# Kernel optimization log

Hardware: AMD Instinct MI355X
Metric: run time of the kernel (lower is better)

The kernel has to match this reference:

```python
import jax, jax.numpy as jnp
import numpy as np

N_NODES = 100000
N_EDGES = 3200000
D_FEAT = 512
D_HID = 64
D_LAT = 16
N_CLASS = 10
N_FLOW = 10
K_PROP = 10
ALPHA_TELEPORT = 0.1


def setup_inputs() -> dict:
    key = jax.random.key(0)
    ks = jax.random.split(key, 8)
    x = jax.random.normal(ks[0], (N_NODES, D_FEAT), jnp.float32)
    edge_index = jax.random.randint(ks[1], (2, N_EDGES), 0, N_NODES)
    p_c = jax.random.uniform(ks[2], (N_CLASS,), jnp.float32) + 0.1
    p_c = p_c / p_c.sum()
    W1 = jax.random.normal(ks[3], (D_FEAT, D_HID), jnp.float32) / np.sqrt(D_FEAT).astype(np.float32)
    b1 = jnp.zeros((D_HID,), jnp.float32)
    W2 = jax.random.normal(ks[4], (D_HID, D_LAT), jnp.float32) / np.sqrt(D_HID).astype(np.float32)
    b2 = jnp.zeros((D_LAT,), jnp.float32)
    flow_z0 = jax.random.normal(ks[5], (N_FLOW, N_CLASS, D_LAT), jnp.float32) * 0.1
    flow_alpha_prime = jax.random.normal(ks[6], (N_FLOW, N_CLASS, 1), jnp.float32) * 0.1
    flow_beta = jax.random.normal(ks[7], (N_FLOW, N_CLASS, 1), jnp.float32) * 0.1
    return dict(x=x, edge_index=edge_index, p_c=p_c, W1=W1, b1=b1, W2=W2, b2=b2,
                flow_z0=flow_z0, flow_alpha_prime=flow_alpha_prime, flow_beta=flow_beta)


def _batched_radial_log_prob(z, flow_z0, flow_alpha_prime, flow_beta):
    # Per-class batched radial flow (invertible pyro-style parameterization).
    # z: [N, D] -> log_q: [N, C]
    C, D = flow_z0.shape[1], flow_z0.shape[2]
    zz = jnp.broadcast_to(z[None], (C, z.shape[0], D))  # [C, N, D]
    sum_logdet = jnp.zeros((C, z.shape[0]), z.dtype)
    for l in range(flow_z0.shape[0]):  # small fixed number of flow layers
        z0 = flow_z0[l][:, None, :]                               # [C,1,D]
        alpha = jax.nn.softplus(flow_alpha_prime[l])[:, None, :]  # [C,1,1]
        beta_hat = -alpha + jax.nn.softplus(flow_beta[l])[:, None, :]
        dz = zz - z0
        r = jnp.sqrt(jnp.sum(dz * dz, axis=-1, keepdims=True))    # [C,N,1]
        h = 1.0 / (alpha + r)
        bh = beta_hat * h
        zz = zz + bh * dz
        logdet = (D - 1) * jnp.log1p(bh) + jnp.log1p(bh - beta_hat * r * h * h)
        sum_logdet = sum_logdet + logdet[..., 0]
    log_base = -0.5 * jnp.sum(zz * zz, axis=-1) - 0.5 * D * jnp.log(2.0 * jnp.pi)
    return (log_base + sum_logdet).T  # [N, C]


def _appnp(beta_ft, edge_index, n_nodes):
    # APPNP with self loops and symmetric gcn normalization over edge list.
    src = jnp.concatenate([edge_index[0], jnp.arange(n_nodes)])
    dst = jnp.concatenate([edge_index[1], jnp.arange(n_nodes)])
    deg = jax.ops.segment_sum(jnp.ones_like(src, dtype=beta_ft.dtype), dst, num_segments=n_nodes)
    dinv = jnp.where(deg > 0, jax.lax.rsqrt(jnp.maximum(deg, 1.0)), 0.0)
    norm = (dinv[src] * dinv[dst])[:, None]  # [E+N, 1]
    x0 = beta_ft
    b = beta_ft
    for _ in range(K_PROP):
        agg = jax.ops.segment_sum(norm * b[src], dst, num_segments=n_nodes)
        b = (1.0 - ALPHA_TELEPORT) * agg + ALPHA_TELEPORT * x0
    return b


def reference(x, edge_index, p_c, W1, b1, W2, b2, flow_z0, flow_alpha_prime, flow_beta):
    h = jax.nn.relu(x @ W1 + b1)           # input_encoder (dropout inactive at eval)
    z = h @ W2 + b2                        # latent_encoder, [N, D_LAT]
    log_q = _batched_radial_log_prob(z, flow_z0, flow_alpha_prime, flow_beta)
    log_q_per_class = log_q + jnp.log(p_c)[None, :]
    log_scale = 0.5 * D_LAT * jnp.log(4.0 * jnp.pi)  # 'latent-new' evidence scale
    beta_ft = jnp.exp(jnp.clip(log_q_per_class + log_scale, -30.0, 30.0))
    beta = _appnp(beta_ft, edge_index, x.shape[0])
    alpha = 1.0 + beta
    soft = alpha / jnp.sum(alpha, axis=-1, keepdims=True)
    hard = jnp.argmax(soft, axis=-1)
    return hard[:, None], soft
```

## Files before the change

kernel.cpp:

```cpp
#include <hip/hip_runtime.h>
#include <math.h>
#include <limits.h>

#define DF 512
#define DH 64
#define DL 16
#define NC 10
#define NF 10
#define KPROP 10

#define BSH 7
#define BW  (1 << BSH)
#define MAXB 1024
#define TILE 16384

__device__ __forceinline__ float softplus_(float x){
  return fmaxf(x, 0.0f) + log1pf(expf(-fabsf(x)));
}

__device__ __forceinline__ unsigned int f2bf_(float f){
  unsigned int u = __float_as_uint(f);
  return (u + 0x7FFFu + ((u >> 16) & 1u)) >> 16;
}
__device__ __forceinline__ unsigned int pack2bf_(float lo, float hi){
  return f2bf_(lo) | (f2bf_(hi) << 16);
}

#define BM 64
#define BN 64
#define BK 32
__global__ __launch_bounds__(256) void k_gemm1z(const float* __restrict__ x,
    const float* __restrict__ W1, const float* __restrict__ b1,
    const float* __restrict__ W2, const float* __restrict__ b2,
    float* __restrict__ z, int N)
{
  __shared__ float smem[2*BK*(BM+4)];
  float (*At)[BM+4] = (float(*)[BM+4])smem;
  float (*Bs)[BN+4] = (float(*)[BN+4])(smem + BK*(BM+4));
  __shared__ float W2s[DH][DL];
  __shared__ float b2s[DL];
  const int tid = threadIdx.x;
  for (int i = tid; i < DH*DL; i += 256) W2s[i>>4][i&15] = W2[i];
  if (tid < DL) b2s[tid] = b2[tid];
  const int tx = tid & 15, ty = tid >> 4;
  const int row0 = blockIdx.x * BM;
  float acc[4][4] = {};
  for (int k0 = 0; k0 < DF; k0 += BK) {
    #pragma unroll
    for (int i = 0; i < 2; ++i) {
      int idx = tid + i*256;
      int r  = idx >> 3;
      int kk = (idx & 7) << 2;
      int row = row0 + r;
      float4 va = make_float4(0.f,0.f,0.f,0.f);
      if (row < N) va = *(const float4*)&x[(size_t)row*DF + k0 + kk];
      At[kk+0][r]=va.x; At[kk+1][r]=va.y; At[kk+2][r]=va.z; At[kk+3][r]=va.w;
      int r2 = idx >> 4;
      int c4 = (idx & 15) << 2;
      float4 vb = *(const float4*)&W1[(size_t)(k0+r2)*DH + c4];
      Bs[r2][c4+0]=vb.x; Bs[r2][c4+1]=vb.y; Bs[r2][c4+2]=vb.z; Bs[r2][c4+3]=vb.w;
    }
    __syncthreads();
    #pragma unroll
    for (int kk = 0; kk < BK; ++kk) {
      float4 av = *(const float4*)&At[kk][ty<<2];
      float4 bv = *(const float4*)&Bs[kk][tx<<2];
      float a4[4]={av.x,av.y,av.z,av.w};
      float b4[4]={bv.x,bv.y,bv.z,bv.w};
      #pragma unroll
      for (int i=0;i<4;++i)
        #pragma unroll
        for (int j=0;j<4;++j) acc[i][j] = fmaf(a4[i], b4[j], acc[i][j]);
    }
    __syncthreads();
  }
  float4 bias = ((const float4*)b1)[tx];
  float bias4[4] = {bias.x, bias.y, bias.z, bias.w};
  float (*hs)[BM+4] = (float(*)[BM+4])smem;
  #pragma unroll
  for (int i=0;i<4;++i){
    #pragma unroll
    for (int j=0;j<4;++j)
      hs[(ty<<2)+i][(tx<<2)+j] = fmaxf(acc[i][j] + bias4[j], 0.0f);
  }
  __syncthreads();
  int row = tid >> 2, lg = tid & 3;
  float4 zacc = ((const float4*)b2s)[lg];
  #pragma unroll 8
  for (int k = 0; k < DH; ++k){
    float hv = hs[row][k];
    float4 wv = *(const float4*)&W2s[k][lg<<2];
    zacc.x = fmaf(hv, wv.x, zacc.x);
    zacc.y = fmaf(hv, wv.y, zacc.y);
    zacc.z = fmaf(hv, wv.z, zacc.z);
    zacc.w = fmaf(hv, wv.w, zacc.w);
  }
  int grow = row0 + row;
  if (grow < N) ((float4*)z)[(size_t)grow*4 + lg] = zacc;
}

__global__ __launch_bounds__(256) void k_flow2(const float* __restrict__ z,
    const float* __restrict__ pc, const float* __restrict__ z0g,
    const float* __restrict__ apg, const float* __restrict__ fbg,
    const float* __restrict__ dinv,
    float* __restrict__ x0, unsigned short* __restrict__ c0b,
    float* __restrict__ y0, int N)
{
  __shared__ float z0s[NF][NC][DL];
  __shared__ float alps[NF][NC];
  __shared__ float bhs[NF][NC];
  __shared__ float lpc[NC];
  int tid = threadIdx.x;
  for (int i = tid; i < NF*NC*DL; i += 256)
    z0s[(i>>4)/NC][(i>>4)%NC][i&15] = z0g[i];
  if (tid < NF*NC){
    int l = tid/NC, c = tid%NC;
    float al = softplus_(apg[tid]);
    alps[l][c] = al;
    bhs[l][c]  = -al + softplus_(fbg[tid]);
  }
  if (tid < NC) lpc[tid] = __logf(pc[tid]);
  __syncthreads();

  int idx = blockIdx.x*256 + tid;
  int n = idx >> 4, c = idx & 15;
  if (n >= N) return;
  float dn = dinv[n];
  if (c >= NC){ x0[idx] = 0.f; c0b[idx] = 0; y0[idx] = 0.f; return; }

  float zz[DL];
  const float4* z4 = (const float4*)z;
  #pragma unroll
  for (int q=0; q<4; ++q){
    float4 v = z4[(size_t)n*4 + q];
    zz[q*4+0]=v.x; zz[q*4+1]=v.y; zz[q*4+2]=v.z; zz[q*4+3]=v.w;
  }
  const float NEGHALFD_LOG2PI = -14.703016531274762f;
  const float LOGSCALE        =  20.248193975754326f;
  float sld = 0.f;
  #pragma unroll 1
  for (int l=0; l<NF; ++l){
    float al = alps[l][c], bhat = bhs[l][c];
    float dz[DL]; float r2 = 0.f;
    #pragma unroll
    for (int d=0; d<DL; ++d){ float t = zz[d] - z0s[l][c][d]; dz[d]=t; r2 = fmaf(t,t,r2); }
    float r  = sqrtf(r2);
    float hh = 1.0f/(al + r);
    float bh = bhat*hh;
    #pragma unroll
    for (int d=0; d<DL; ++d) zz[d] = fmaf(bh, dz[d], zz[d]);
    sld += 15.0f*__logf(1.0f + bh) + __logf(1.0f + bh - bhat*r*hh*hh);
  }
  float q2 = 0.f;
  #pragma unroll
  for (int d=0; d<DL; ++d) q2 = fmaf(zz[d], zz[d], q2);
  float v = -0.5f*q2 + NEGHALFD_LOG2PI + sld + lpc[c] + LOGSCALE;
  v = fminf(fmaxf(v, -30.f), 30.f);
  float xv = __expf(v);
  x0[idx] = xv;
  float cv = dn*xv;
  c0b[idx] = (unsigned short)f2bf_(cv);
  y0[idx]  = 0.1f*cv;
}

__global__ __launch_bounds__(256) void k_bhist(const int* __restrict__ dst,
    int* __restrict__ bCnt, int E, int B)
{
  __shared__ int hh[MAXB];
  int tid = threadIdx.x;
  for (int b = tid; b < B; b += 256) hh[b] = 0;
  __syncthreads();
  for (int i = blockIdx.x*256 + tid; i < E; i += gridDim.x*256)
    atomicAdd(&hh[dst[i] >> BSH], 1);
  __syncthreads();
  for (int b = tid; b < B; b += 256) if (hh[b]) atomicAdd(&bCnt[b], hh[b]);
}

__global__ __launch_bounds__(256) void k_scan_small(const int* __restrict__ in,
    int* __restrict__ out, int n, int writeTotal)
{
  __shared__ int sd[1024];
  int tid = threadIdx.x;
  int orig[4];
  #pragma unroll
  for (int j = 0; j < 4; ++j){
    int i = tid + j*256;
    orig[j] = (i < n) ? in[i] : 0;
    sd[i] = orig[j];
  }
  __syncthreads();
  for (int ofs = 1; ofs < 1024; ofs <<= 1){
    int vals[4];
    #pragma unroll
    for (int j = 0; j < 4; ++j){
      int i = tid + j*256;
      vals[j] = (i >= ofs) ? sd[i-ofs] : 0;
    }
    __syncthreads();
    #pragma unroll
    for (int j = 0; j < 4; ++j) sd[tid + j*256] += vals[j];
    __syncthreads();
  }
  #pragma unroll
  for (int j = 0; j < 4; ++j){
    int i = tid + j*256;
    if (i < n) out[i] = sd[i] - orig[j];
  }
  if (writeTotal && tid == 0) out[n] = sd[n-1];
}

__global__ __launch_bounds__(256) void k_bscatter(const int* __restrict__ src,
    const int* __restrict__ dst, const int* __restrict__ bOff,
    int* __restrict__ bCur, int* __restrict__ bp, int E, int B)
{
  __shared__ int hc[MAXB];
  __shared__ int hb[MAXB];
  int tid = threadIdx.x;
  int base = blockIdx.x * TILE;
  int lim  = base + TILE; if (lim > E) lim = E;
  for (int b = tid; b < B; b += 256) hc[b] = 0;
  __syncthreads();
  for (int i = base + tid; i < lim; i += 256)
    atomicAdd(&hc[dst[i] >> BSH], 1);
  __syncthreads();
  for (int b = tid; b < B; b += 256){
    int c = hc[b];
    hb[b] = c ? atomicAdd(&bCur[b], c) : 0;
    hc[b] = 0;
  }
  __syncthreads();
  for (int i = base + tid; i < lim; i += 256){
    int d = dst[i];
    int b = d >> BSH;
    int pos = bOff[b] + hb[b] + atomicAdd(&hc[b], 1);
    bp[pos] = (src[i] << BSH) | (d & (BW-1));
  }
}

__global__ __launch_bounds__(256) void k_bdeg(const int* __restrict__ bp,
    const int* __restrict__ bOff, int* __restrict__ deg,
    float* __restrict__ dinv, float* __restrict__ dinv2, int N)
{
  __shared__ int cur[BW];
  int tid = threadIdx.x;
  int b = blockIdx.x;
  if (tid < BW) cur[tid] = 0;
  __syncthreads();
  int s = bOff[b], e = bOff[b+1];
  for (int i = s + tid; i < e; i += 256)
    atomicAdd(&cur[bp[i] & (BW-1)], 1);
  __syncthreads();
  int node = (b << BSH) + tid;
  if (tid < BW && node < N){
    int d = cur[tid] + 1;
    deg[node] = d;
    float dv = 1.0f / sqrtf((float)d);
    dinv[node]  = dv;
    dinv2[node] = dv*dv;
  }
}

__global__ __launch_bounds__(256) void k_scan_part(const int* __restrict__ deg,
    int* __restrict__ part, int N){
  __shared__ int sd[256];
  int base = blockIdx.x*1024;
  int tid = threadIdx.x;
  int s = 0;
  #pragma unroll
  for (int i=0;i<4;++i){ int idx = base + tid*4 + i; if (idx < N) s += deg[idx]; }
  sd[tid] = s; __syncthreads();
  for (int ofs=128; ofs>0; ofs>>=1){ if (tid<ofs) sd[tid]+=sd[tid+ofs]; __syncthreads(); }
  if (tid==0) part[blockIdx.x] = sd[0];
}

__global__ __launch_bounds__(256) void k_scan_final(const int* __restrict__ deg,
    const int* __restrict__ part, int* __restrict__ off, int N, int E)
{
  __shared__ int sc[256];
  int base = blockIdx.x*1024;
  int tid = threadIdx.x;
  int v[4]; int s = 0;
  #pragma unroll
  for (int i=0;i<4;++i){ int idx = base + tid*4 + i; v[i] = (idx<N)?deg[idx]:0; s += v[i]; }
  sc[tid] = s; __syncthreads();
  for (int ofs=1; ofs<256; ofs<<=1){
    int t = (tid>=ofs) ? sc[tid-ofs] : 0;
    __syncthreads();
    sc[tid] += t;
    __syncthreads();
  }
  int ex = sc[tid] - s + part[blockIdx.x];
  #pragma unroll
  for (int i=0;i<4;++i){
    int idx = base + tid*4 + i;
    if (idx < N){
      off[idx] = ex;
      if (idx == N-1) off[N] = ex + v[i];
      ex += v[i];
    }
  }
}

__global__ __launch_bounds__(256) void k_place(const int* __restrict__ bp,
    const int* __restrict__ bOff, const int* __restrict__ off,
    int* __restrict__ csr, int N)
{
  __shared__ int cur[BW];
  int tid = threadIdx.x;
  int b = blockIdx.x;
  int node0 = b << BSH;
  if (tid < BW){
    cur[tid] = 1;
    int node = node0 + tid;
    if (node < N) csr[off[node]] = node;
  }
  __syncthreads();
  int s = bOff[b], e = bOff[b+1];
  for (int i = s + tid; i < e; i += 256){
    int v  = bp[i];
    int dl = v & (BW-1);
    int sn = v >> BSH;
    int d  = node0 + dl;
    int p  = off[d] + atomicAdd(&cur[dl], 1);
    csr[p] = sn;
  }
}

__global__ __launch_bounds__(256) void k_rank(int* __restrict__ csr,
    const int* __restrict__ off, int N)
{
  int wid  = (blockIdx.x*256 + threadIdx.x) >> 6;
  int lane = threadIdx.x & 63;
  if (wid >= N) return;
  int s = off[wid], e = off[wid+1];
  int d = e - s;
  if (d <= 1) return;
  if (d <= 64){
    int v = (lane < d) ? csr[s+lane] : INT_MAX;
    int rank = 0;
    for (int j = 0; j < d; ++j){
      int bv = __shfl(v, j);
      rank += (bv < v) || (bv == v && j < lane);
    }
    if (lane < d) csr[s+rank] = v;
  } else if (d <= 256){
    int v0 = (lane      < d) ? csr[s+lane      ] : INT_MAX;
    int v1 = (lane+64   < d) ? csr[s+lane+64   ] : INT_MAX;
    int v2 = (lane+128  < d) ? csr[s+lane+128  ] : INT_MAX;
    int v3 = (lane+192  < d) ? csr[s+lane+192  ] : INT_MAX;
    int r0=0,r1=0,r2=0,r3=0;
    for (int j = 0; j < d; ++j){
      int slot = j >> 6, jl = j & 63;
      int bv = (slot==0) ? __shfl(v0,jl) : (slot==1) ? __shfl(v1,jl)
             : (slot==2) ? __shfl(v2,jl) : __shfl(v3,jl);
      r0 += (bv < v0) || (bv == v0 && j < lane);
      r1 += (bv < v1) || (bv == v1 && j < lane+64);
      r2 += (bv < v2) || (bv == v2 && j < lane+128);
      r3 += (bv < v3) || (bv == v3 && j < lane+192);
    }
    if (lane      < d) csr[s+r0]=v0;
    if (lane+64   < d) csr[s+r1]=v1;
    if (lane+128  < d) csr[s+r2]=v2;
    if (lane+192  < d) csr[s+r3]=v3;
  } else {
    if (lane == 0){
      for (int i = s+1; i < e; ++i){
        int key = csr[i]; int j = i-1;
        while (j >= s && csr[j] > key){ csr[j+1] = csr[j]; --j; }
        csr[j+1] = key;
      }
    }
  }
}

__global__ __launch_bounds__(256) void k_prop(const uint4* __restrict__ cin,
    const float* __restrict__ y0, const float* __restrict__ dinv2,
    uint4* __restrict__ cout,
    const int* __restrict__ csr, const int* __restrict__ off, int N)
{
  int t = blockIdx.x*256 + threadIdx.x;
  int n = t >> 3, sub = t & 7, qh = sub >> 2, part = sub & 3;
  if (n >= N) return;
  int s = off[n], e = off[n+1], d = e - s;
  int lo = s + ((d*part) >> 2);
  int hi = s + ((d*(part+1)) >> 2);
  float a[8] = {0.f,0.f,0.f,0.f,0.f,0.f,0.f,0.f};
  float b[8] = {0.f,0.f,0.f,0.f,0.f,0.f,0.f,0.f};
  int i = lo;
  for (; i+2 <= hi; i += 2){
    int s0 = csr[i], s1 = csr[i+1];
    uint4 u0 = cin[(size_t)s0*2 + qh];
    uint4 u1 = cin[(size_t)s1*2 + qh];
    a[0] += __uint_as_float(u0.x << 16); a[1] += __uint_as_float(u0.x & 0xFFFF0000u);
    a[2] += __uint_as_float(u0.y << 16); a[3] += __uint_as_float(u0.y & 0xFFFF0000u);
    a[4] += __uint_as_float(u0.z << 16); a[5] += __uint_as_float(u0.z & 0xFFFF0000u);
    a[6] += __uint_as_float(u0.w << 16); a[7] += __uint_as_float(u0.w & 0xFFFF0000u);
    b[0] += __uint_as_float(u1.x << 16); b[1] += __uint_as_float(u1.x & 0xFFFF0000u);
    b[2] += __uint_as_float(u1.y << 16); b[3] += __uint_as_float(u1.y & 0xFFFF0000u);
    b[4] += __uint_as_float(u1.z << 16); b[5] += __uint_as_float(u1.z & 0xFFFF0000u);
    b[6] += __uint_as_float(u1.w << 16); b[7] += __uint_as_float(u1.w & 0xFFFF0000u);
  }
  if (i < hi){
    uint4 u0 = cin[(size_t)csr[i]*2 + qh];
    a[0] += __uint_as_float(u0.x << 16); a[1] += __uint_as_float(u0.x & 0xFFFF0000u);
    a[2] += __uint_as_float(u0.y << 16); a[3] += __uint_as_float(u0.y & 0xFFFF0000u);
    a[4] += __uint_as_float(u0.z << 16); a[5] += __uint_as_float(u0.z & 0xFFFF0000u);
    a[6] += __uint_as_float(u0.w << 16); a[7] += __uint_as_float(u0.w & 0xFFFF0000u);
  }
  float v[8];
  #pragma unroll
  for (int j = 0; j < 8; ++j){
    float t2 = a[j] + b[j];
    t2 += __shfl_xor(t2, 1, 4);
    t2 += __shfl_xor(t2, 2, 4);
    v[j] = t2;
  }
  if (part == 0){
    float w9 = 0.9f * dinv2[n];
    const float4* y4 = (const float4*)y0;
    float4 ya = y4[(size_t)n*4 + qh*2];
    float4 yb = y4[(size_t)n*4 + qh*2 + 1];
    float o0 = fmaf(w9, v[0], ya.x), o1 = fmaf(w9, v[1], ya.y);
    float o2 = fmaf(w9, v[2], ya.z), o3 = fmaf(w9, v[3], ya.w);
    float o4 = fmaf(w9, v[4], yb.x), o5 = fmaf(w9, v[5], yb.y);
    float o6 = fmaf(w9, v[6], yb.z), o7 = fmaf(w9, v[7], yb.w);
    uint4 w;
    w.x = pack2bf_(o0, o1); w.y = pack2bf_(o2, o3);
    w.z = pack2bf_(o4, o5); w.w = pack2bf_(o6, o7);
    cout[(size_t)n*2 + qh] = w;
  }
}

__global__ __launch_bounds__(256) void k_prop_final(const uint4* __restrict__ cin,
    const float* __restrict__ x0, const float* __restrict__ dinv,
    const int* __restrict__ csr, const int* __restrict__ off,
    float* __restrict__ out, int N)
{
  int t = blockIdx.x*256 + threadIdx.x;
  int n = t >> 3, sub = t & 7, qh = sub >> 2, part = sub & 3;
  if (n >= N) return;
  int s = off[n], e = off[n+1], d = e - s;
  int lo = s + ((d*part) >> 2);
  int hi = s + ((d*(part+1)) >> 2);
  float a[8] = {0.f,0.f,0.f,0.f,0.f,0.f,0.f,0.f};
  float b[8] = {0.f,0.f,0.f,0.f,0.f,0.f,0.f,0.f};
  int i = lo;
  for (; i+2 <= hi; i += 2){
    int s0 = csr[i], s1 = csr[i+1];
    uint4 u0 = cin[(size_t)s0*2 + qh];
    uint4 u1 = cin[(size_t)s1*2 + qh];
    a[0] += __uint_as_float(u0.x << 16); a[1] += __uint_as_float(u0.x & 0xFFFF0000u);
    a[2] += __uint_as_float(u0.y << 16); a[3] += __uint_as_float(u0.y & 0xFFFF0000u);
    a[4] += __uint_as_float(u0.z << 16); a[5] += __uint_as_float(u0.z & 0xFFFF0000u);
    a[6] += __uint_as_float(u0.w << 16); a[7] += __uint_as_float(u0.w & 0xFFFF0000u);
    b[0] += __uint_as_float(u1.x << 16); b[1] += __uint_as_float(u1.x & 0xFFFF0000u);
    b[2] += __uint_as_float(u1.y << 16); b[3] += __uint_as_float(u1.y & 0xFFFF0000u);
    b[4] += __uint_as_float(u1.z << 16); b[5] += __uint_as_float(u1.z & 0xFFFF0000u);
    b[6] += __uint_as_float(u1.w << 16); b[7] += __uint_as_float(u1.w & 0xFFFF0000u);
  }
  if (i < hi){
    uint4 u0 = cin[(size_t)csr[i]*2 + qh];
    a[0] += __uint_as_float(u0.x << 16); a[1] += __uint_as_float(u0.x & 0xFFFF0000u);
    a[2] += __uint_as_float(u0.y << 16); a[3] += __uint_as_float(u0.y & 0xFFFF0000u);
    a[4] += __uint_as_float(u0.z << 16); a[5] += __uint_as_float(u0.z & 0xFFFF0000u);
    a[6] += __uint_as_float(u0.w << 16); a[7] += __uint_as_float(u0.w & 0xFFFF0000u);
  }
  float v[8];
  #pragma unroll
  for (int j = 0; j < 8; ++j){
    float t2 = a[j] + b[j];
    t2 += __shfl_xor(t2, 1, 4);
    t2 += __shfl_xor(t2, 2, 4);
    v[j] = t2;
  }
  if (part != 0) return;

  float w9 = 0.9f * dinv[n];
  const float4* x4 = (const float4*)x0;
  float4 xa = x4[(size_t)n*4 + qh*2];
  float4 xb = x4[(size_t)n*4 + qh*2 + 1];
  float xv[8] = {xa.x, xa.y, xa.z, xa.w, xb.x, xb.y, xb.z, xb.w};
  float al[8];
  #pragma unroll
  for (int j = 0; j < 8; ++j) al[j] = fmaf(w9, v[j], fmaf(0.1f, xv[j], 1.f));

  int nv = qh ? 2 : 8;
  float sv = 0.f;
  for (int j = 0; j < nv; ++j) sv += al[j];
  sv += __shfl_xor(sv, 4, 8);

  float bv = -1e30f; int bi = 999;
  for (int j = 0; j < nv; ++j){
    if (al[j] > bv){ bv = al[j]; bi = qh*8 + j; }
  }
  {
    float vo = __shfl_xor(bv, 4, 8);
    int  io  = __shfl_xor(bi, 4, 8);
    if (vo > bv || (vo == bv && io < bi)){ bv = vo; bi = io; }
  }

  float inv = 1.0f / sv;
  size_t sb = (size_t)N + (size_t)n*NC;
  for (int j = 0; j < nv; ++j) out[sb + qh*8 + j] = al[j] * inv;
  if (sub == 0) out[n] = (float)bi;
}

extern "C" void kernel_launch(void* const* d_in, const int* in_sizes, int n_in,
                              void* d_out, int out_size, void* d_ws, size_t ws_size,
                              hipStream_t stream)
{
  const float* x  = (const float*)d_in[0];
  const int*   ei = (const int*)  d_in[1];
  const float* pc = (const float*)d_in[2];
  const float* W1 = (const float*)d_in[3];
  const float* b1 = (const float*)d_in[4];
  const float* W2 = (const float*)d_in[5];
  const float* b2 = (const float*)d_in[6];
  const float* z0 = (const float*)d_in[7];
  const float* ap = (const float*)d_in[8];
  const float* fb = (const float*)d_in[9];
  float* out = (float*)d_out;

  const int N = in_sizes[0] / DF;
  const int E = in_sizes[1] / 2;
  const int* src = ei;
  const int* dst = ei + E;
  const int B = (N + BW - 1) >> BSH;

  char* ws = (char*)d_ws;
  size_t o = 0;
  size_t region0 = (size_t)E*sizeof(int);
  if ((size_t)N*DL*sizeof(float) > region0) region0 = (size_t)N*DL*sizeof(float);
  int*   bp   = (int*)  (ws + o);
  float* z    = (float*)(ws + o);
  o += region0;
  int*   csr  = (int*)  (ws + o); o += (size_t)(E+N)*sizeof(int);
  float* x0   = (float*)(ws + o); o += (size_t)N*DL*sizeof(float);
  float* y0   = (float*)(ws + o); o += (size_t)N*DL*sizeof(float);
  unsigned short* c0b = (unsigned short*)(ws + o); o += (size_t)N*DL*2;
  unsigned short* cAb = (unsigned short*)(ws + o); o += (size_t)N*DL*2;
  unsigned short* cBb = (unsigned short*)(ws + o); o += (size_t)N*DL*2;
  int*   deg  = (int*)  (ws + o); o += (size_t)N*sizeof(int);
  float* dinv = (float*)(ws + o); o += (size_t)N*sizeof(float);
  float* dinv2= (float*)(ws + o); o += (size_t)N*sizeof(float);
  int*   offs = (int*)  (ws + o); o += (size_t)(N+2)*sizeof(int);
  int*   part = (int*)  (ws + o); o += 4096;
  int*   bCnt = (int*)  (ws + o); o += MAXB*sizeof(int);
  int*   bOff = (int*)  (ws + o); o += (MAXB+1)*sizeof(int);
  int*   bCur = (int*)  (ws + o); o += MAXB*sizeof(int);

  const int TB = 256;
  int nb  = (N + 1023) / 1024;

  hipMemsetAsync(bCnt, 0, MAXB*sizeof(int), stream);
  hipMemsetAsync(bCur, 0, MAXB*sizeof(int), stream);
  k_bhist<<<512, TB, 0, stream>>>(dst, bCnt, E, B);
  k_scan_small<<<1, TB, 0, stream>>>(bCnt, bOff, B, 1);
  k_bscatter<<<(E + TILE - 1)/TILE, TB, 0, stream>>>(src, dst, bOff, bCur, bp, E, B);
  k_bdeg<<<B, TB, 0, stream>>>(bp, bOff, deg, dinv, dinv2, N);
  k_scan_part<<<nb, TB, 0, stream>>>(deg, part, N);
  k_scan_small<<<1, TB, 0, stream>>>(part, part, nb, 0);
  k_scan_final<<<nb, TB, 0, stream>>>(deg, part, offs, N, E);
  k_place<<<B, TB, 0, stream>>>(bp, bOff, offs, csr, N);
  k_rank<<<(N + 3) / 4, TB, 0, stream>>>(csr, offs, N);

  k_gemm1z<<<(N + BM - 1) / BM, TB, 0, stream>>>(x, W1, b1, W2, b2, z, N);
  k_flow2<<<((N*DL) + TB - 1) / TB, TB, 0, stream>>>(z, pc, z0, ap, fb, dinv,
                                                     x0, c0b, y0, N);

  int gP = ((N*8) + TB - 1) / TB;
  const unsigned short* cin = c0b;
  for (int it = 0; it < KPROP-1; ++it){
    unsigned short* cout = (it & 1) ? cBb : cAb;
    k_prop<<<gP, TB, 0, stream>>>((const uint4*)cin, y0, dinv2,
                                  (uint4*)cout, csr, offs, N);
    cin = cout;
  }
  k_prop_final<<<gP, TB, 0, stream>>>((const uint4*)cin, x0, dinv,
                                      csr, offs, out, N);
}
```

Measured before the change: 647.2 us.

## Process nodes in degree-sorted order in propagation kernels for load balance

Builds a degree histogram while computing node degrees, scans it, and counting-sorts the node ids by degree into a permutation. The propagation kernels then map thread groups to nodes through this permutation, so wavefronts handle nodes of similar degree and lose less time to divergence. The cost is an extra histogram, scan and scatter pass, plus an indirection that makes the per-node y0 reads and output writes non-contiguous.

```diff
diff --git a/kernel.cpp b/kernel.cpp
--- a/kernel.cpp
+++ b/kernel.cpp
@@ -239,12 +239,15 @@
 
 __global__ __launch_bounds__(256) void k_bdeg(const int* __restrict__ bp,
     const int* __restrict__ bOff, int* __restrict__ deg,
-    float* __restrict__ dinv, float* __restrict__ dinv2, int N)
+    float* __restrict__ dinv, float* __restrict__ dinv2,
+    int* __restrict__ dH, int N)
 {
   __shared__ int cur[BW];
+  __shared__ int lh[256];
   int tid = threadIdx.x;
   int b = blockIdx.x;
   if (tid < BW) cur[tid] = 0;
+  lh[tid] = 0;
   __syncthreads();
   int s = bOff[b], e = bOff[b+1];
   for (int i = s + tid; i < e; i += 256)
@@ -257,7 +260,23 @@
     float dv = 1.0f / sqrtf((float)d);
     dinv[node]  = dv;
     dinv2[node] = dv*dv;
-  }
+    int dc = d < 255 ? d : 255;
+    atomicAdd(&lh[dc], 1);
+  }
+  __syncthreads();
+  if (lh[tid]) atomicAdd(&dH[tid], lh[tid]);
+}
+
+__global__ __launch_bounds__(256) void k_permscatter(const int* __restrict__ deg,
+    const int* __restrict__ dHo, int* __restrict__ dHc,
+    int* __restrict__ perm, int N)
+{
+  int n = blockIdx.x*256 + threadIdx.x;
+  if (n >= N) return;
+  int d = deg[n];
+  int dc = d < 255 ? d : 255;
+  int pos = dHo[dc] + atomicAdd(&dHc[dc], 1);
+  perm[pos] = n;
 }
 
 __global__ __launch_bounds__(256) void k_scan_part(const int* __restrict__ deg,
@@ -375,12 +394,13 @@
 
 __global__ __launch_bounds__(256) void k_prop(const uint4* __restrict__ cin,
     const float* __restrict__ y0, const float* __restrict__ dinv2,
-    uint4* __restrict__ cout,
-    const int* __restrict__ csr, const int* __restrict__ off, int N)
+    uint4* __restrict__ cout, const int* __restrict__ csr,
+    const int* __restrict__ off, const int* __restrict__ perm, int N)
 {
   int t = blockIdx.x*256 + threadIdx.x;
-  int n = t >> 3, sub = t & 7, qh = sub >> 2, part = sub & 3;
-  if (n >= N) return;
+  int g = t >> 3, sub = t & 7, qh = sub >> 2, part = sub & 3;
+  if (g >= N) return;
+  int n = perm[g];
   int s = off[n], e = off[n+1], d = e - s;
   int lo = s + ((d*part) >> 2);
   int hi = s + ((d*(part+1)) >> 2);
@@ -434,11 +454,12 @@
 __global__ __launch_bounds__(256) void k_prop_final(const uint4* __restrict__ cin,
     const float* __restrict__ x0, const float* __restrict__ dinv,
     const int* __restrict__ csr, const int* __restrict__ off,
-    float* __restrict__ out, int N)
+    const int* __restrict__ perm, float* __restrict__ out, int N)
 {
   int t = blockIdx.x*256 + threadIdx.x;
-  int n = t >> 3, sub = t & 7, qh = sub >> 2, part = sub & 3;
-  if (n >= N) return;
+  int g = t >> 3, sub = t & 7, qh = sub >> 2, part = sub & 3;
+  if (g >= N) return;
+  int n = perm[g];
   int s = off[n], e = off[n+1], d = e - s;
   int lo = s + ((d*part) >> 2);
   int hi = s + ((d*(part+1)) >> 2);
@@ -541,6 +562,7 @@
   unsigned short* cAb = (unsigned short*)(ws + o); o += (size_t)N*DL*2;
   unsigned short* cBb = (unsigned short*)(ws + o); o += (size_t)N*DL*2;
   int*   deg  = (int*)  (ws + o); o += (size_t)N*sizeof(int);
+  int*   perm = (int*)  (ws + o); o += (size_t)N*sizeof(int);
   float* dinv = (float*)(ws + o); o += (size_t)N*sizeof(float);
   float* dinv2= (float*)(ws + o); o += (size_t)N*sizeof(float);
   int*   offs = (int*)  (ws + o); o += (size_t)(N+2)*sizeof(int);
@@ -548,16 +570,24 @@
   int*   bCnt = (int*)  (ws + o); o += MAXB*sizeof(int);
   int*   bOff = (int*)  (ws + o); o += (MAXB+1)*sizeof(int);
   int*   bCur = (int*)  (ws + o); o += MAXB*sizeof(int);
+  int*   dH   = (int*)  (ws + o); o += 256*sizeof(int);
+  int*   dHo  = (int*)  (ws + o); o += 257*sizeof(int);
+  int*   dHc  = (int*)  (ws + o); o += 256*sizeof(int);
 
   const int TB = 256;
+  int gN  = (N + TB - 1) / TB;
   int nb  = (N + 1023) / 1024;
 
   hipMemsetAsync(bCnt, 0, MAXB*sizeof(int), stream);
   hipMemsetAsync(bCur, 0, MAXB*sizeof(int), stream);
+  hipMemsetAsync(dH,   0, 256*sizeof(int), stream);
+  hipMemsetAsync(dHc,  0, 256*sizeof(int), stream);
   k_bhist<<<512, TB, 0, stream>>>(dst, bCnt, E, B);
   k_scan_small<<<1, TB, 0, stream>>>(bCnt, bOff, B, 1);
   k_bscatter<<<(E + TILE - 1)/TILE, TB, 0, stream>>>(src, dst, bOff, bCur, bp, E, B);
-  k_bdeg<<<B, TB, 0, stream>>>(bp, bOff, deg, dinv, dinv2, N);
+  k_bdeg<<<B, TB, 0, stream>>>(bp, bOff, deg, dinv, dinv2, dH, N);
+  k_scan_small<<<1, TB, 0, stream>>>(dH, dHo, 256, 1);
+  k_permscatter<<<gN, TB, 0, stream>>>(deg, dHo, dHc, perm, N);
   k_scan_part<<<nb, TB, 0, stream>>>(deg, part, N);
   k_scan_small<<<1, TB, 0, stream>>>(part, part, nb, 0);
   k_scan_final<<<nb, TB, 0, stream>>>(deg, part, offs, N, E);
@@ -573,9 +603,9 @@
   for (int it = 0; it < KPROP-1; ++it){
     unsigned short* cout = (it & 1) ? cBb : cAb;
     k_prop<<<gP, TB, 0, stream>>>((const uint4*)cin, y0, dinv2,
-                                  (uint4*)cout, csr, offs, N);
+                                  (uint4*)cout, csr, offs, perm, N);
     cin = cout;
   }
   k_prop_final<<<gP, TB, 0, stream>>>((const uint4*)cin, x0, dinv,
-                                      csr, offs, out, N);
-}
+                                      csr, offs, perm, out, N);
+}
```

Result: slower. 972.4 us (+50.2%).
